# Optimization experiments

Measured on AMD Instinct MI355X. Metric: run time of the kernel, lower is better.

Reference implementation:

```python
import jax, jax.numpy as jnp
import numpy as np

N = 100000
E = 1600000
F_IN = 128
DIM = 32
NUM_CLASSES = 40
BN_EPS = 1e-5


def setup_inputs() -> dict:
    key = jax.random.key(0)
    ks = jax.random.split(key, 16)
    inp = {}
    inp['x'] = jax.random.normal(ks[0], (N, F_IN), dtype=jnp.float32)
    inp['edge_index'] = jax.random.randint(ks[1], (2, E), 0, N, dtype=jnp.int64)
    s = lambda fan_in: 1.0 / np.sqrt(fan_in)
    # GINConv 1 MLP: Linear(F_IN, DIM) -> ReLU -> Linear(DIM, DIM)
    inp['w1a'] = jax.random.uniform(ks[2], (F_IN, DIM), jnp.float32, -s(F_IN), s(F_IN))
    inp['b1a'] = jnp.zeros((DIM,), jnp.float32)
    inp['w1b'] = jax.random.uniform(ks[3], (DIM, DIM), jnp.float32, -s(DIM), s(DIM))
    inp['b1b'] = jnp.zeros((DIM,), jnp.float32)
    # GINConv 2 MLP: Linear(DIM, DIM) -> ReLU -> Linear(DIM, DIM)
    inp['w2a'] = jax.random.uniform(ks[4], (DIM, DIM), jnp.float32, -s(DIM), s(DIM))
    inp['b2a'] = jnp.zeros((DIM,), jnp.float32)
    inp['w2b'] = jax.random.uniform(ks[5], (DIM, DIM), jnp.float32, -s(DIM), s(DIM))
    inp['b2b'] = jnp.zeros((DIM,), jnp.float32)
    # BatchNorm params (eval mode: running stats)
    inp['bn1_g'] = jnp.ones((DIM,), jnp.float32)
    inp['bn1_b'] = jnp.zeros((DIM,), jnp.float32)
    inp['bn1_m'] = jax.random.normal(ks[6], (DIM,), jnp.float32) * 0.1
    inp['bn1_v'] = jax.random.uniform(ks[7], (DIM,), jnp.float32, 0.5, 1.5)
    inp['bn2_g'] = jnp.ones((DIM,), jnp.float32)
    inp['bn2_b'] = jnp.zeros((DIM,), jnp.float32)
    inp['bn2_m'] = jax.random.normal(ks[8], (DIM,), jnp.float32) * 0.1
    inp['bn2_v'] = jax.random.uniform(ks[9], (DIM,), jnp.float32, 0.5, 1.5)
    # FC heads
    inp['fc1_w'] = jax.random.uniform(ks[10], (DIM, DIM), jnp.float32, -s(DIM), s(DIM))
    inp['fc1_b'] = jnp.zeros((DIM,), jnp.float32)
    inp['fc2_w'] = jax.random.uniform(ks[11], (DIM, NUM_CLASSES), jnp.float32, -s(DIM), s(DIM))
    inp['fc2_b'] = jnp.zeros((NUM_CLASSES,), jnp.float32)
    return inp


def _gin_conv(x, src, dst, wa, ba, wb, bb):
    # sum-aggregate neighbor features (messages flow src -> dst), eps = 0
    agg = jax.ops.segment_sum(x[src], dst, num_segments=N)
    h = agg + x  # (1 + eps) * x + sum_j x_j
    h = jax.nn.relu(h @ wa + ba)
    return h @ wb + bb


def _bn(x, g, b, m, v):
    return (x - m) * (g * jax.lax.rsqrt(v + BN_EPS)) + b


def reference(x, edge_index, w1a, b1a, w1b, b1b, w2a, b2a, w2b, b2b,
              bn1_g, bn1_b, bn1_m, bn1_v, bn2_g, bn2_b, bn2_m, bn2_v,
              fc1_w, fc1_b, fc2_w, fc2_b):
    src, dst = edge_index[0], edge_index[1]
    h = jax.nn.relu(_gin_conv(x, src, dst, w1a, b1a, w1b, b1b))
    h = _bn(h, bn1_g, bn1_b, bn1_m, bn1_v)  # dropout is identity in eval
    h = _gin_conv(h, src, dst, w2a, b2a, w2b, b2b)
    h = _bn(h, bn2_g, bn2_b, bn2_m, bn2_v)
    h = jax.nn.relu(h @ fc1_w + fc1_b)
    logits = h @ fc2_w + fc2_b
    return jax.nn.log_softmax(logits, axis=1)
```

## Files before the change

### kernel.cpp

```cpp
#include <hip/hip_runtime.h>
#include <hip/hip_bf16.h>

static constexpr int N_   = 100000;
static constexpr int E_   = 1600000;
static constexpr int FIN_ = 128;
static constexpr int DIM_ = 32;
static constexpr int NC_  = 40;
static constexpr int NB_BKT = (N_ + 127) / 128;
static constexpr int NCHUNK = 256;
static constexpr int EPC    = E_ / NCHUNK;
static constexpr int PROJ_NB = N_ / 32;
static constexpr int CS_NB  = (NB_BKT + 7) / 8;

__device__ __forceinline__ int edge_at(const void* e, int is64, long long i) {
    return is64 ? (int)((const long long*)e)[i] : ((const int*)e)[i];
}

__device__ __forceinline__ float bflo(unsigned u) { return __uint_as_float(u << 16); }
__device__ __forceinline__ float bfhi(unsigned u) { return __uint_as_float(u & 0xffff0000u); }

#define DETECT_FLAG(edge, sflag)                                        \
    if (threadIdx.x < 64) {                                             \
        const long long* p_ = (const long long*)(edge);                 \
        long long v_ = p_[threadIdx.x];                                 \
        bool bad_ = (v_ < 0 || v_ >= (long long)N_);                    \
        unsigned long long m_ = __ballot(bad_);                         \
        if (threadIdx.x == 0) sflag = (m_ == 0ull) ? 1 : 0;             \
    }                                                                   \
    __syncthreads();

__global__ __launch_bounds__(256) void chist_kernel(const void* __restrict__ edge,
                                                    int* __restrict__ ghist) {
    __shared__ int lh[NB_BKT];
    __shared__ int sflag;
    DETECT_FLAG(edge, sflag)
    for (int i = threadIdx.x; i < NB_BKT; i += 256) lh[i] = 0;
    __syncthreads();
    int f = sflag;
    int b = blockIdx.x;
    int end = b * EPC + EPC;
    for (int e = b * EPC + threadIdx.x; e < end; e += 256) {
        int d = edge_at(edge, f, (long long)E_ + e);
        atomicAdd(&lh[d >> 7], 1);
    }
    __syncthreads();
    for (int i = threadIdx.x; i < NB_BKT; i += 256) ghist[b * NB_BKT + i] = lh[i];
}

__global__ __launch_bounds__(256) void colscan_kernel(const int* __restrict__ ghist,
                                                      int* __restrict__ gcur,
                                                      int* __restrict__ bcnt,
                                                      int* __restrict__ bbase,
                                                      int* __restrict__ offs,
                                                      int* __restrict__ done) {
    __shared__ int tile[256 * 9];
    __shared__ int a[256];
    __shared__ int lastFlag;
    int tid = threadIdx.x;
    int k0 = blockIdx.x * 8;

    {
        int kk = tid & 7, r0 = tid >> 3;
        for (int p = 0; p < 8; ++p) {
            int b = r0 + p * 32;
            int k = k0 + kk;
            tile[b * 9 + kk] = (k < NB_BKT) ? ghist[b * NB_BKT + k] : 0;
        }
    }
    __syncthreads();

    int c = tid >> 5, lane = tid & 31;
    int v[8]; int s = 0;
#pragma unroll
    for (int r = 0; r < 8; ++r) { v[r] = tile[(lane * 8 + r) * 9 + c]; s += v[r]; }
    int incl = s;
#pragma unroll
    for (int off = 1; off < 32; off <<= 1) {
        int u = __shfl_up(incl, off, 32);
        if (lane >= off) incl += u;
    }
    int ex = incl - s;
    int k = k0 + c;
    if (k < NB_BKT) {
        int run = ex;
#pragma unroll
        for (int r = 0; r < 8; ++r) {
            int b = lane * 8 + r;
            gcur[b * NB_BKT + k] = run;
            run += v[r];
        }
        if (lane == 31) bcnt[k] = run;
    }
    __syncthreads();
    if (tid == 0) {
        __threadfence();
        int old = atomicAdd(done, 1);
        lastFlag = (old == CS_NB - 1) ? 1 : 0;
    }
    __syncthreads();
    if (lastFlag) {
        __threadfence();
        int b4[4]; int base4 = tid * 4; int t = 0;
#pragma unroll
        for (int j = 0; j < 4; ++j) { int i = base4 + j; b4[j] = (i < NB_BKT) ? bcnt[i] : 0; t += b4[j]; }
        a[tid] = t;
        __syncthreads();
        for (int off = 1; off < 256; off <<= 1) {
            int u = a[tid] + ((tid >= off) ? a[tid - off] : 0);
            __syncthreads(); a[tid] = u; __syncthreads();
        }
        int g = a[tid] - t;
#pragma unroll
        for (int j = 0; j < 4; ++j) { int i = base4 + j; if (i < NB_BKT) bbase[i] = g; g += b4[j]; }
        if (tid == 255) offs[N_] = a[255];
    }
}

__global__ __launch_bounds__(256) void dscatter_kernel(const void* __restrict__ edge,
                                                       const int* __restrict__ bbase,
                                                       const int* __restrict__ gcur,
                                                       int* __restrict__ packed) {
    __shared__ int cur[NB_BKT];
    __shared__ int sflag;
    DETECT_FLAG(edge, sflag)
    int b = blockIdx.x, tid = threadIdx.x;
    for (int k = tid; k < NB_BKT; k += 256) cur[k] = bbase[k] + gcur[b * NB_BKT + k];
    __syncthreads();
    int f = sflag;
    int end = b * EPC + EPC;
    for (int e = b * EPC + tid; e < end; e += 256) {
        int s = edge_at(edge, f, e);
        int d = edge_at(edge, f, (long long)E_ + e);
        int pos = atomicAdd(&cur[d >> 7], 1);
        packed[pos] = s | ((d & 127) << 17);
    }
}

__global__ __launch_bounds__(256) void fat_kernel(const int* __restrict__ bcnt,
                                                  const int* __restrict__ bbase,
                                                  const int* __restrict__ packed,
                                                  int* __restrict__ offs,
                                                  int* __restrict__ csr,
                                                  const float* __restrict__ x,
                                                  const float* __restrict__ w,
                                                  __hip_bfloat16* __restrict__ yh) {
    __shared__ __align__(16) char smem[32768];
    int tid = threadIdx.x;
    if (blockIdx.x < NB_BKT) {
        int* c   = (int*)smem;
        int* cur = (int*)smem + 128;
        int b = blockIdx.x;
        int beg = bbase[b], cnt = bcnt[b];
        if (tid < 128) c[tid] = 0;
        __syncthreads();
        for (int i = tid; i < cnt; i += 256)
            atomicAdd(&c[packed[beg + i] >> 17], 1);
        __syncthreads();
        int myv = (tid < 128) ? c[tid] : 0;
        for (int off = 1; off < 128; off <<= 1) {
            int t = 0;
            if (tid < 128) t = c[tid] + ((tid >= off) ? c[tid - off] : 0);
            __syncthreads();
            if (tid < 128) c[tid] = t;
            __syncthreads();
        }
        if (tid < 128) {
            int ex = c[tid] - myv;
            cur[tid] = ex;
            int node = b * 128 + tid;
            if (node < N_) offs[node] = beg + ex;
        }
        __syncthreads();
        for (int i = tid; i < cnt; i += 256) {
            int v = packed[beg + i];
            int p = atomicAdd(&cur[v >> 17], 1);
            csr[beg + p] = v & 0x1FFFF;
        }
    } else {
        float* wsm = (float*)smem;
        float* xs  = (float*)(smem + 16384);
        const float4* w4 = (const float4*)w;
        float4* ws4 = (float4*)wsm;
        for (int i = tid; i < FIN_ * DIM_ / 4; i += 256) ws4[i] = w4[i];

        int nodeBase = (blockIdx.x - NB_BKT) * 32;
        const float4* x4 = (const float4*)(x + (size_t)nodeBase * FIN_);
        float4* xs4 = (float4*)xs;
        for (int i = tid; i < 32 * FIN_ / 4; i += 256) xs4[i] = x4[i];
        __syncthreads();

        int d = tid & 31, ns = tid >> 5;
        for (int rep = 0; rep < 4; ++rep) {
            int node = ns + rep * 8;
            float acc = 0.f;
#pragma unroll 4
            for (int k = 0; k < FIN_; ++k) acc += xs[node * FIN_ + k] * wsm[k * DIM_ + d];
            yh[(size_t)(nodeBase + node) * DIM_ + d] = __float2bfloat16(acc);
        }
    }
}

__device__ __forceinline__ void gather_row(const int* __restrict__ csr,
                                           const char* __restrict__ vb,
                                           int beg, int end, int loff,
                                           float& a0, float& a1, float& a2, float& a3) {
    int i = beg;
    for (; i + 3 < end; i += 4) {
        int s0 = csr[i], s1 = csr[i + 1], s2 = csr[i + 2], s3 = csr[i + 3];
        uint2 u0 = *(const uint2*)(vb + (((size_t)s0) << 6) + loff);
        uint2 u1 = *(const uint2*)(vb + (((size_t)s1) << 6) + loff);
        uint2 u2 = *(const uint2*)(vb + (((size_t)s2) << 6) + loff);
        uint2 u3 = *(const uint2*)(vb + (((size_t)s3) << 6) + loff);
        a0 += (bflo(u0.x) + bflo(u1.x)) + (bflo(u2.x) + bflo(u3.x));
        a1 += (bfhi(u0.x) + bfhi(u1.x)) + (bfhi(u2.x) + bfhi(u3.x));
        a2 += (bflo(u0.y) + bflo(u1.y)) + (bflo(u2.y) + bflo(u3.y));
        a3 += (bfhi(u0.y) + bfhi(u1.y)) + (bfhi(u2.y) + bfhi(u3.y));
    }
    for (; i < end; ++i) {
        int s0 = csr[i];
        uint2 u0 = *(const uint2*)(vb + (((size_t)s0) << 6) + loff);
        a0 += bflo(u0.x); a1 += bfhi(u0.x); a2 += bflo(u0.y); a3 += bfhi(u0.y);
    }
}

__global__ __launch_bounds__(256) void aggmlp1_kernel(const int* __restrict__ offs,
                                                      const int* __restrict__ csr,
                                                      const __hip_bfloat16* __restrict__ yh,
                                                      const float* __restrict__ b1a,
                                                      const float* __restrict__ w1b,
                                                      const float* __restrict__ b1b,
                                                      const float* __restrict__ g1,
                                                      const float* __restrict__ be1,
                                                      const float* __restrict__ m1,
                                                      const float* __restrict__ v1,
                                                      const float* __restrict__ w2a,
                                                      __hip_bfloat16* __restrict__ zh) {
    __shared__ float A[32 * 33];
    __shared__ float B[32 * 33];
    __shared__ float w1s[DIM_ * DIM_];
    __shared__ float w2s[DIM_ * DIM_];
    int tid = threadIdx.x;
    for (int i = tid; i < DIM_ * DIM_; i += 256) { w1s[i] = w1b[i]; w2s[i] = w2a[i]; }

    int nl = tid >> 3, lane = tid & 7;
    int node = blockIdx.x * 32 + nl;
    int beg = offs[node], end = offs[node + 1];
    float a0 = 0.f, a1 = 0.f, a2 = 0.f, a3 = 0.f;
    gather_row(csr, (const char*)yh, beg, end, lane << 3, a0, a1, a2, a3);
    {
        float* p = &A[nl * 33 + lane * 4];
        p[0] = a0; p[1] = a1; p[2] = a2; p[3] = a3;
    }
    __syncthreads();

    int d = tid & 31, ng = tid >> 5;
    size_t gbase = (size_t)blockIdx.x * 32 * DIM_;

#pragma unroll
    for (int r = 0; r < 4; ++r) {
        int n = r * 8 + ng;
        float yv = __bfloat162float(yh[gbase + n * DIM_ + d]);
        A[n * 33 + d] = fmaxf(A[n * 33 + d] + yv + b1a[d], 0.f);
    }
    __syncthreads();

    float sc1 = g1[d] * rsqrtf(v1[d] + 1e-5f);
    float sh1 = be1[d] - m1[d] * sc1;

#pragma unroll
    for (int r = 0; r < 4; ++r) {
        int n = r * 8 + ng;
        float s = b1b[d];
#pragma unroll
        for (int k = 0; k < DIM_; ++k) s += A[n * 33 + k] * w1s[k * DIM_ + d];
        B[n * 33 + d] = fmaxf(s, 0.f) * sc1 + sh1;
    }
    __syncthreads();

#pragma unroll
    for (int r = 0; r < 4; ++r) {
        int n = r * 8 + ng;
        float s = 0.f;
#pragma unroll
        for (int k = 0; k < DIM_; ++k) s += B[n * 33 + k] * w2s[k * DIM_ + d];
        zh[gbase + n * DIM_ + d] = __float2bfloat16(s);
    }
}

__global__ __launch_bounds__(256) void aggmlp2_kernel(const int* __restrict__ offs,
                                                      const int* __restrict__ csr,
                                                      const __hip_bfloat16* __restrict__ zh,
                                                      const float* __restrict__ b2a,
                                                      const float* __restrict__ w2b,
                                                      const float* __restrict__ b2b,
                                                      const float* __restrict__ g2,
                                                      const float* __restrict__ be2,
                                                      const float* __restrict__ m2,
                                                      const float* __restrict__ v2,
                                                      const float* __restrict__ f1w,
                                                      const float* __restrict__ f1b,
                                                      const float* __restrict__ f2w,
                                                      const float* __restrict__ f2b,
                                                      float* __restrict__ out) {
    __shared__ float A[32 * 33];
    __shared__ float BC[DIM_ * NC_];
    __shared__ float wA[DIM_ * DIM_];
    __shared__ float wB[DIM_ * DIM_];
    int tid = threadIdx.x;
    for (int i = tid; i < DIM_ * DIM_; i += 256) { wA[i] = w2b[i]; wB[i] = f1w[i]; }

    int nl = tid >> 3, lane = tid & 7;
    int node = blockIdx.x * 32 + nl;
    int beg = offs[node], end = offs[node + 1];
    float a0 = 0.f, a1 = 0.f, a2 = 0.f, a3 = 0.f;
    gather_row(csr, (const char*)zh, beg, end, lane << 3, a0, a1, a2, a3);
    {
        float* p = &A[nl * 33 + lane * 4];
        p[0] = a0; p[1] = a1; p[2] = a2; p[3] = a3;
    }
    __syncthreads();

    int d = tid & 31, ng = tid >> 5;
    size_t gbase = (size_t)blockIdx.x * 32 * DIM_;

#pragma unroll
    for (int r = 0; r < 4; ++r) {
        int n = r * 8 + ng;
        float zv = __bfloat162float(zh[gbase + n * DIM_ + d]);
        A[n * 33 + d] = fmaxf(A[n * 33 + d] + zv + b2a[d], 0.f);
    }
    __syncthreads();

    float sc2 = g2[d] * rsqrtf(v2[d] + 1e-5f);
    float sh2 = be2[d] - m2[d] * sc2;

#pragma unroll
    for (int r = 0; r < 4; ++r) {
        int n = r * 8 + ng;
        float s = b2b[d];
#pragma unroll
        for (int k = 0; k < DIM_; ++k) s += A[n * 33 + k] * wA[k * DIM_ + d];
        BC[n * 33 + d] = s * sc2 + sh2;
    }
    __syncthreads();

#pragma unroll
    for (int r = 0; r < 4; ++r) {
        int n = r * 8 + ng;
        float s = f1b[d];
#pragma unroll
        for (int k = 0; k < DIM_; ++k) s += BC[n * 33 + k] * wB[k * DIM_ + d];
        A[n * 33 + d] = fmaxf(s, 0.f);
    }
    __syncthreads();
    for (int i = tid; i < DIM_ * NC_; i += 256) BC[i] = f2w[i];
    __syncthreads();

    int c2 = 32 + (d & 7);
#pragma unroll
    for (int r = 0; r < 4; ++r) {
        int n = r * 8 + ng;
        float l0 = f2b[d];
        float l1 = f2b[c2];
#pragma unroll
        for (int k = 0; k < DIM_; ++k) {
            float fv = A[n * 33 + k];
            l0 += fv * BC[k * NC_ + d];
            l1 += fv * BC[k * NC_ + c2];
        }
        float mx = fmaxf(l0, l1);
#pragma unroll
        for (int off = 16; off; off >>= 1) mx = fmaxf(mx, __shfl_xor(mx, off));
        float se = __expf(l0 - mx) + ((d < 8) ? __expf(l1 - mx) : 0.f);
#pragma unroll
        for (int off = 16; off; off >>= 1) se += __shfl_xor(se, off);
        float lse = mx + __logf(se);
        size_t ob = (size_t)(blockIdx.x * 32 + n) * NC_;
        out[ob + d] = l0 - lse;
        if (d < 8) out[ob + 32 + d] = l1 - lse;
    }
}

extern "C" void kernel_launch(void* const* d_in, const int* in_sizes, int n_in,
                              void* d_out, int out_size, void* d_ws, size_t ws_size,
                              hipStream_t stream) {
    const float* x   = (const float*)d_in[0];
    const void*  edg = d_in[1];
    const float* w1a = (const float*)d_in[2];
    const float* b1a = (const float*)d_in[3];
    const float* w1b = (const float*)d_in[4];
    const float* b1b = (const float*)d_in[5];
    const float* w2a = (const float*)d_in[6];
    const float* b2a = (const float*)d_in[7];
    const float* w2b = (const float*)d_in[8];
    const float* b2b = (const float*)d_in[9];
    const float* g1  = (const float*)d_in[10];
    const float* be1 = (const float*)d_in[11];
    const float* m1  = (const float*)d_in[12];
    const float* v1  = (const float*)d_in[13];
    const float* g2  = (const float*)d_in[14];
    const float* be2 = (const float*)d_in[15];
    const float* m2  = (const float*)d_in[16];
    const float* v2  = (const float*)d_in[17];
    const float* f1w = (const float*)d_in[18];
    const float* f1b = (const float*)d_in[19];
    const float* f2w = (const float*)d_in[20];
    const float* f2b = (const float*)d_in[21];
    float* out = (float*)d_out;

    char* ws = (char*)d_ws;
    int* done   = (int*)ws;
    int* bcnt   = (int*)(ws + 256);
    int* bbase  = (int*)(ws + 3584);
    int* ghist  = (int*)(ws + 6912);
    int* gcur   = (int*)(ws + 807680);
    int* offs   = (int*)(ws + 1608448);
    int* packed = (int*)(ws + 2008576);
    int* csr    = (int*)(ws + 8408576);
    __hip_bfloat16* yh = (__hip_bfloat16*)(ws + 14808576);
    __hip_bfloat16* zh = (__hip_bfloat16*)(ws + 21208576);

    hipMemsetAsync(done, 0, 4, stream);

    chist_kernel<<<NCHUNK, 256, 0, stream>>>(edg, ghist);
    colscan_kernel<<<CS_NB, 256, 0, stream>>>(ghist, gcur, bcnt, bbase, offs, done);
    dscatter_kernel<<<NCHUNK, 256, 0, stream>>>(edg, bbase, gcur, packed);
    fat_kernel<<<NB_BKT + PROJ_NB, 256, 0, stream>>>(bcnt, bbase, packed, offs, csr,
                                                     x, w1a, yh);

    aggmlp1_kernel<<<N_ / 32, 256, 0, stream>>>(offs, csr, yh, b1a, w1b, b1b,
                                                g1, be1, m1, v1, w2a, zh);

    aggmlp2_kernel<<<N_ / 32, 256, 0, stream>>>(offs, csr, zh, b2a, w2b, b2b,
                                                g2, be2, m2, v2, f1w, f1b,
                                                f2w, f2b, out);
}
```

Before: 324.5 us.

## Fuse CSR build kernels with grid barriers; sort gather lanes by degree

```diff
diff --git a/kernel.cpp b/kernel.cpp
--- a/kernel.cpp
+++ b/kernel.cpp
@@ -10,7 +10,7 @@
 static constexpr int NCHUNK = 256;
 static constexpr int EPC    = E_ / NCHUNK;
 static constexpr int PROJ_NB = N_ / 32;
-static constexpr int CS_NB  = (NB_BKT + 7) / 8;
+static constexpr int CS_TASKS = (NB_BKT + 7) / 8;
 
 __device__ __forceinline__ int edge_at(const void* e, int is64, long long i) {
     return is64 ? (int)((const long long*)e)[i] : ((const int*)e)[i];
@@ -19,120 +19,134 @@
 __device__ __forceinline__ float bflo(unsigned u) { return __uint_as_float(u << 16); }
 __device__ __forceinline__ float bfhi(unsigned u) { return __uint_as_float(u & 0xffff0000u); }
 
-#define DETECT_FLAG(edge, sflag)                                        \
-    if (threadIdx.x < 64) {                                             \
-        const long long* p_ = (const long long*)(edge);                 \
-        long long v_ = p_[threadIdx.x];                                 \
-        bool bad_ = (v_ < 0 || v_ >= (long long)N_);                    \
-        unsigned long long m_ = __ballot(bad_);                         \
-        if (threadIdx.x == 0) sflag = (m_ == 0ull) ? 1 : 0;             \
-    }                                                                   \
-    __syncthreads();
-
-__global__ __launch_bounds__(256) void chist_kernel(const void* __restrict__ edge,
-                                                    int* __restrict__ ghist) {
-    __shared__ int lh[NB_BKT];
+__device__ __forceinline__ void grid_barrier(int* cnt, int* gen, int phase) {
+    __syncthreads();
+    if (threadIdx.x == 0) {
+        __threadfence();
+        int old = atomicAdd(cnt, 1);
+        if (old == phase * NCHUNK - 1) {
+            __threadfence();
+            atomicExch(gen, phase);
+        } else {
+            while (atomicAdd(gen, 0) < phase) { __builtin_amdgcn_s_sleep(1); }
+        }
+        __threadfence();
+    }
+    __syncthreads();
+}
+
+__global__ __launch_bounds__(512) void mega_kernel(const void* __restrict__ edge,
+                                                   int* __restrict__ ghist,
+                                                   int* __restrict__ gcur,
+                                                   int* __restrict__ bcnt,
+                                                   int* __restrict__ bbase,
+                                                   int* __restrict__ offs,
+                                                   int* __restrict__ packed,
+                                                   int* __restrict__ bar) {
+    __shared__ int smem[2816];
     __shared__ int sflag;
-    DETECT_FLAG(edge, sflag)
-    for (int i = threadIdx.x; i < NB_BKT; i += 256) lh[i] = 0;
+    int tid = threadIdx.x;
+    int b = blockIdx.x;
+
+    if (tid < 64) {
+        const long long* p_ = (const long long*)edge;
+        long long v_ = p_[tid];
+        bool bad_ = (v_ < 0 || v_ >= (long long)N_);
+        unsigned long long m_ = __ballot(bad_);
+        if (tid == 0) sflag = (m_ == 0ull) ? 1 : 0;
+    }
     __syncthreads();
     int f = sflag;
-    int b = blockIdx.x;
-    int end = b * EPC + EPC;
-    for (int e = b * EPC + threadIdx.x; e < end; e += 256) {
-        int d = edge_at(edge, f, (long long)E_ + e);
-        atomicAdd(&lh[d >> 7], 1);
-    }
-    __syncthreads();
-    for (int i = threadIdx.x; i < NB_BKT; i += 256) ghist[b * NB_BKT + i] = lh[i];
-}
-
-__global__ __launch_bounds__(256) void colscan_kernel(const int* __restrict__ ghist,
-                                                      int* __restrict__ gcur,
-                                                      int* __restrict__ bcnt,
-                                                      int* __restrict__ bbase,
-                                                      int* __restrict__ offs,
-                                                      int* __restrict__ done) {
-    __shared__ int tile[256 * 9];
-    __shared__ int a[256];
-    __shared__ int lastFlag;
-    int tid = threadIdx.x;
-    int k0 = blockIdx.x * 8;
-
+
+    int* lh = smem;
+    for (int i = tid; i < NB_BKT; i += 512) lh[i] = 0;
+    __syncthreads();
     {
-        int kk = tid & 7, r0 = tid >> 3;
-        for (int p = 0; p < 8; ++p) {
-            int b = r0 + p * 32;
-            int k = k0 + kk;
-            tile[b * 9 + kk] = (k < NB_BKT) ? ghist[b * NB_BKT + k] : 0;
-        }
-    }
-    __syncthreads();
-
-    int c = tid >> 5, lane = tid & 31;
-    int v[8]; int s = 0;
-#pragma unroll
-    for (int r = 0; r < 8; ++r) { v[r] = tile[(lane * 8 + r) * 9 + c]; s += v[r]; }
-    int incl = s;
-#pragma unroll
-    for (int off = 1; off < 32; off <<= 1) {
-        int u = __shfl_up(incl, off, 32);
-        if (lane >= off) incl += u;
-    }
-    int ex = incl - s;
-    int k = k0 + c;
-    if (k < NB_BKT) {
-        int run = ex;
-#pragma unroll
-        for (int r = 0; r < 8; ++r) {
-            int b = lane * 8 + r;
-            gcur[b * NB_BKT + k] = run;
-            run += v[r];
-        }
-        if (lane == 31) bcnt[k] = run;
-    }
-    __syncthreads();
-    if (tid == 0) {
-        __threadfence();
-        int old = atomicAdd(done, 1);
-        lastFlag = (old == CS_NB - 1) ? 1 : 0;
-    }
-    __syncthreads();
-    if (lastFlag) {
-        __threadfence();
-        int b4[4]; int base4 = tid * 4; int t = 0;
-#pragma unroll
-        for (int j = 0; j < 4; ++j) { int i = base4 + j; b4[j] = (i < NB_BKT) ? bcnt[i] : 0; t += b4[j]; }
-        a[tid] = t;
+        int end = b * EPC + EPC;
+        for (int e = b * EPC + tid; e < end; e += 512) {
+            int d = edge_at(edge, f, (long long)E_ + e);
+            atomicAdd(&lh[d >> 7], 1);
+        }
+    }
+    __syncthreads();
+    for (int i = tid; i < NB_BKT; i += 512) ghist[b * NB_BKT + i] = lh[i];
+    grid_barrier(bar, bar + 1, 1);
+
+    if (b < CS_TASKS) {
+        int* tile = smem;
+        int k0 = b * 8;
+        {
+            int kk = tid & 7, r0 = tid >> 3;
+            for (int p = 0; p < 4; ++p) {
+                int bb = r0 + p * 64;
+                int k = k0 + kk;
+                tile[bb * 9 + kk] = (k < NB_BKT) ? ghist[bb * NB_BKT + k] : 0;
+            }
+        }
+        __syncthreads();
+        if (tid < 256) {
+            int c = tid >> 5, lane = tid & 31;
+            int v[8]; int s = 0;
+#pragma unroll
+            for (int r = 0; r < 8; ++r) { v[r] = tile[(lane * 8 + r) * 9 + c]; s += v[r]; }
+            int incl = s;
+#pragma unroll
+            for (int off = 1; off < 32; off <<= 1) {
+                int u = __shfl_up(incl, off, 32);
+                if (lane >= off) incl += u;
+            }
+            int ex = incl - s;
+            int k = k0 + c;
+            if (k < NB_BKT) {
+                int run = ex;
+#pragma unroll
+                for (int r = 0; r < 8; ++r) {
+                    int bb = lane * 8 + r;
+                    gcur[bb * NB_BKT + k] = run;
+                    run += v[r];
+                }
+                if (lane == 31) bcnt[k] = run;
+            }
+        }
+    }
+    grid_barrier(bar, bar + 1, 2);
+
+    if (b == 0) {
+        int* a = smem;
+        int b4[4]; int base4 = tid * 4; int t4 = 0;
+        if (tid < 256) {
+#pragma unroll
+            for (int j = 0; j < 4; ++j) { int i = base4 + j; b4[j] = (i < NB_BKT) ? bcnt[i] : 0; t4 += b4[j]; }
+            a[tid] = t4;
+        }
         __syncthreads();
         for (int off = 1; off < 256; off <<= 1) {
-            int u = a[tid] + ((tid >= off) ? a[tid - off] : 0);
-            __syncthreads(); a[tid] = u; __syncthreads();
-        }
-        int g = a[tid] - t;
-#pragma unroll
-        for (int j = 0; j < 4; ++j) { int i = base4 + j; if (i < NB_BKT) bbase[i] = g; g += b4[j]; }
+            int u = 0;
+            if (tid < 256) u = a[tid] + ((tid >= off) ? a[tid - off] : 0);
+            __syncthreads();
+            if (tid < 256) a[tid] = u;
+            __syncthreads();
+        }
+        if (tid < 256) {
+            int g = a[tid] - t4;
+#pragma unroll
+            for (int j = 0; j < 4; ++j) { int i = base4 + j; if (i < NB_BKT) bbase[i] = g; g += b4[j]; }
+        }
         if (tid == 255) offs[N_] = a[255];
     }
-}
-
-__global__ __launch_bounds__(256) void dscatter_kernel(const void* __restrict__ edge,
-                                                       const int* __restrict__ bbase,
-                                                       const int* __restrict__ gcur,
-                                                       int* __restrict__ packed) {
-    __shared__ int cur[NB_BKT];
-    __shared__ int sflag;
-    DETECT_FLAG(edge, sflag)
-    int b = blockIdx.x, tid = threadIdx.x;
-    for (int k = tid; k < NB_BKT; k += 256) cur[k] = bbase[k] + gcur[b * NB_BKT + k];
-    __syncthreads();
-    int f = sflag;
-    int end = b * EPC + EPC;
-    for (int e = b * EPC + tid; e < end; e += 256) {
-        int s = edge_at(edge, f, e);
-        int d = edge_at(edge, f, (long long)E_ + e);
-        int pos = atomicAdd(&cur[d >> 7], 1);
-        packed[pos] = s | ((d & 127) << 17);
+    grid_barrier(bar, bar + 1, 3);
+
+    int* cur = smem;
+    for (int k = tid; k < NB_BKT; k += 512) cur[k] = bbase[k] + gcur[b * NB_BKT + k];
+    __syncthreads();
+    {
+        int end = b * EPC + EPC;
+        for (int e = b * EPC + tid; e < end; e += 512) {
+            int s = edge_at(edge, f, e);
+            int d = edge_at(edge, f, (long long)E_ + e);
+            int pos = atomicAdd(&cur[d >> 7], 1);
+            packed[pos] = s | ((d & 127) << 17);
+        }
     }
 }
 
@@ -206,7 +220,10 @@
                                            float& a0, float& a1, float& a2, float& a3) {
     int i = beg;
     for (; i + 3 < end; i += 4) {
-        int s0 = csr[i], s1 = csr[i + 1], s2 = csr[i + 2], s3 = csr[i + 3];
+        int s0 = __builtin_nontemporal_load(csr + i);
+        int s1 = __builtin_nontemporal_load(csr + i + 1);
+        int s2 = __builtin_nontemporal_load(csr + i + 2);
+        int s3 = __builtin_nontemporal_load(csr + i + 3);
         uint2 u0 = *(const uint2*)(vb + (((size_t)s0) << 6) + loff);
         uint2 u1 = *(const uint2*)(vb + (((size_t)s1) << 6) + loff);
         uint2 u2 = *(const uint2*)(vb + (((size_t)s2) << 6) + loff);
@@ -217,11 +234,25 @@
         a3 += (bfhi(u0.y) + bfhi(u1.y)) + (bfhi(u2.y) + bfhi(u3.y));
     }
     for (; i < end; ++i) {
-        int s0 = csr[i];
+        int s0 = __builtin_nontemporal_load(csr + i);
         uint2 u0 = *(const uint2*)(vb + (((size_t)s0) << 6) + loff);
         a0 += bflo(u0.x); a1 += bfhi(u0.x); a2 += bflo(u0.y); a3 += bfhi(u0.y);
     }
 }
+
+#define BUILD_PERM(offs_)                                               \
+    if (tid < 32) degs[tid] = offs_[blockIdx.x * 32 + tid + 1] -        \
+                              offs_[blockIdx.x * 32 + tid];             \
+    __syncthreads();                                                    \
+    if (tid < 32) {                                                     \
+        int mydeg = degs[tid]; int r = 0;                               \
+        for (int j = 0; j < 32; ++j) {                                  \
+            int dj = degs[j];                                           \
+            r += (dj > mydeg) || (dj == mydeg && j < tid);              \
+        }                                                               \
+        perm[(r & 3) * 8 + (r >> 2)] = tid;                             \
+    }                                                                   \
+    __syncthreads();
 
 __global__ __launch_bounds__(256) void aggmlp1_kernel(const int* __restrict__ offs,
                                                       const int* __restrict__ csr,
@@ -239,16 +270,24 @@
     __shared__ float B[32 * 33];
     __shared__ float w1s[DIM_ * DIM_];
     __shared__ float w2s[DIM_ * DIM_];
+    __shared__ int degs[32];
+    __shared__ int perm[32];
     int tid = threadIdx.x;
     for (int i = tid; i < DIM_ * DIM_; i += 256) { w1s[i] = w1b[i]; w2s[i] = w2a[i]; }
 
+    BUILD_PERM(offs)
+
     int nl = tid >> 3, lane = tid & 7;
-    int node = blockIdx.x * 32 + nl;
+    int j = perm[nl];
+    int node = blockIdx.x * 32 + j;
     int beg = offs[node], end = offs[node + 1];
-    float a0 = 0.f, a1 = 0.f, a2 = 0.f, a3 = 0.f;
-    gather_row(csr, (const char*)yh, beg, end, lane << 3, a0, a1, a2, a3);
+    const char* vb = (const char*)yh;
+    int loff = lane << 3;
+    uint2 us = *(const uint2*)(vb + (((size_t)node) << 6) + loff);
+    float a0 = bflo(us.x), a1 = bfhi(us.x), a2 = bflo(us.y), a3 = bfhi(us.y);
+    gather_row(csr, vb, beg, end, loff, a0, a1, a2, a3);
     {
-        float* p = &A[nl * 33 + lane * 4];
+        float* p = &A[j * 33 + lane * 4];
         p[0] = a0; p[1] = a1; p[2] = a2; p[3] = a3;
     }
     __syncthreads();
@@ -259,8 +298,7 @@
 #pragma unroll
     for (int r = 0; r < 4; ++r) {
         int n = r * 8 + ng;
-        float yv = __bfloat162float(yh[gbase + n * DIM_ + d]);
-        A[n * 33 + d] = fmaxf(A[n * 33 + d] + yv + b1a[d], 0.f);
+        A[n * 33 + d] = fmaxf(A[n * 33 + d] + b1a[d], 0.f);
     }
     __syncthreads();
 
@@ -306,28 +344,34 @@
     __shared__ float BC[DIM_ * NC_];
     __shared__ float wA[DIM_ * DIM_];
     __shared__ float wB[DIM_ * DIM_];
+    __shared__ int degs[32];
+    __shared__ int perm[32];
     int tid = threadIdx.x;
     for (int i = tid; i < DIM_ * DIM_; i += 256) { wA[i] = w2b[i]; wB[i] = f1w[i]; }
 
+    BUILD_PERM(offs)
+
     int nl = tid >> 3, lane = tid & 7;
-    int node = blockIdx.x * 32 + nl;
+    int j = perm[nl];
+    int node = blockIdx.x * 32 + j;
     int beg = offs[node], end = offs[node + 1];
-    float a0 = 0.f, a1 = 0.f, a2 = 0.f, a3 = 0.f;
-    gather_row(csr, (const char*)zh, beg, end, lane << 3, a0, a1, a2, a3);
+    const char* vb = (const char*)zh;
+    int loff = lane << 3;
+    uint2 us = *(const uint2*)(vb + (((size_t)node) << 6) + loff);
+    float a0 = bflo(us.x), a1 = bfhi(us.x), a2 = bflo(us.y), a3 = bfhi(us.y);
+    gather_row(csr, vb, beg, end, loff, a0, a1, a2, a3);
     {
-        float* p = &A[nl * 33 + lane * 4];
+        float* p = &A[j * 33 + lane * 4];
         p[0] = a0; p[1] = a1; p[2] = a2; p[3] = a3;
     }
     __syncthreads();
 
     int d = tid & 31, ng = tid >> 5;
-    size_t gbase = (size_t)blockIdx.x * 32 * DIM_;
-
-#pragma unroll
-    for (int r = 0; r < 4; ++r) {
-        int n = r * 8 + ng;
-        float zv = __bfloat162float(zh[gbase + n * DIM_ + d]);
-        A[n * 33 + d] = fmaxf(A[n * 33 + d] + zv + b2a[d], 0.f);
+
+#pragma unroll
+    for (int r = 0; r < 4; ++r) {
+        int n = r * 8 + ng;
+        A[n * 33 + d] = fmaxf(A[n * 33 + d] + b2a[d], 0.f);
     }
     __syncthreads();
 
@@ -376,8 +420,8 @@
         for (int off = 16; off; off >>= 1) se += __shfl_xor(se, off);
         float lse = mx + __logf(se);
         size_t ob = (size_t)(blockIdx.x * 32 + n) * NC_;
-        out[ob + d] = l0 - lse;
-        if (d < 8) out[ob + 32 + d] = l1 - lse;
+        __builtin_nontemporal_store(l0 - lse, &out[ob + d]);
+        if (d < 8) __builtin_nontemporal_store(l1 - lse, &out[ob + 32 + d]);
     }
 }
 
@@ -409,7 +453,7 @@
     float* out = (float*)d_out;
 
     char* ws = (char*)d_ws;
-    int* done   = (int*)ws;
+    int* bar    = (int*)ws;
     int* bcnt   = (int*)(ws + 256);
     int* bbase  = (int*)(ws + 3584);
     int* ghist  = (int*)(ws + 6912);
@@ -420,11 +464,10 @@
     __hip_bfloat16* yh = (__hip_bfloat16*)(ws + 14808576);
     __hip_bfloat16* zh = (__hip_bfloat16*)(ws + 21208576);
 
-    hipMemsetAsync(done, 0, 4, stream);
-
-    chist_kernel<<<NCHUNK, 256, 0, stream>>>(edg, ghist);
-    colscan_kernel<<<CS_NB, 256, 0, stream>>>(ghist, gcur, bcnt, bbase, offs, done);
-    dscatter_kernel<<<NCHUNK, 256, 0, stream>>>(edg, bbase, gcur, packed);
+    hipMemsetAsync(bar, 0, 16, stream);
+
+    mega_kernel<<<NCHUNK, 512, 0, stream>>>(edg, ghist, gcur, bcnt, bbase, offs,
+                                            packed, bar);
     fat_kernel<<<NB_BKT + PROJ_NB, 256, 0, stream>>>(bcnt, bbase, packed, offs, csr,
                                                      x, w1a, yh);
 
```

After: 376.3 us. 15.9% more time.
